# Performance work log

Measured on AMD Instinct MI355X. Metric: run time of the kernel, lower is better.

## Reference

```python
import jax, jax.numpy as jnp
import numpy as np

D_MODEL = 1024
NUM_HEADS = 16
HEAD_DIM = D_MODEL // NUM_HEADS
SCALE = HEAD_DIM ** -0.5
ROPE_BASE = 10000.0


def _rope_cos_sin(seq_len, dim, dtype=jnp.float32):
    inv_freq = 1.0 / (ROPE_BASE ** (jnp.arange(0, dim, 2, dtype=jnp.float32) / dim))
    t = jnp.arange(seq_len, dtype=jnp.float32)
    freqs = t[:, None] * inv_freq[None, :]            # [S, dim/2]
    emb = jnp.concatenate([freqs, freqs], axis=-1)    # [S, dim]
    # broadcast shape [1, S, 1, dim] to apply over [B, S, H, dim]
    return emb.astype(dtype)[None, :, None, :]


def _rotate_half(x):
    half = x.shape[-1] // 2
    x1, x2 = x[..., :half], x[..., half:]
    return jnp.concatenate([-x2, x1], axis=-1)


def setup_inputs() -> dict:
    key = jax.random.key(0)
    ks = jax.random.split(key, 5)
    B, S = 2, 2048
    x = jax.random.normal(ks[0], (B, S, D_MODEL), dtype=jnp.float32)
    wq = jax.random.normal(ks[1], (D_MODEL, D_MODEL), dtype=jnp.float32) * (D_MODEL ** -0.5)
    wk = jax.random.normal(ks[2], (D_MODEL, D_MODEL), dtype=jnp.float32) * (D_MODEL ** -0.5)
    wv = jax.random.normal(ks[3], (D_MODEL, D_MODEL), dtype=jnp.float32) * (D_MODEL ** -0.5)
    wo = jax.random.normal(ks[4], (D_MODEL, D_MODEL), dtype=jnp.float32) * (D_MODEL ** -0.5)
    attention_mask = jnp.tril(jnp.ones((S, S), dtype=jnp.int32))  # causal
    return {"x": x, "wq": wq, "wk": wk, "wv": wv, "wo": wo,
            "attention_mask": attention_mask}


def reference(x, wq, wk, wv, wo, attention_mask):
    B, S, _ = x.shape
    # projections (nn.Linear, no bias: y = x @ W^T)
    q = (x @ wq.T).reshape(B, S, NUM_HEADS, HEAD_DIM)
    k = (x @ wk.T).reshape(B, S, NUM_HEADS, HEAD_DIM)
    v = (x @ wv.T).reshape(B, S, NUM_HEADS, HEAD_DIM)
    # RoPE
    emb = _rope_cos_sin(S, HEAD_DIM, x.dtype)
    cos, sin = jnp.cos(emb), jnp.sin(emb)
    q = q * cos + _rotate_half(q) * sin
    k = k * cos + _rotate_half(k) * sin
    # attention scores [B, H, S, S]
    scores = jnp.einsum('bihd,bjhd->bhij', q, k) * SCALE
    mask = attention_mask[None, None, :, :]  # 2D mask -> broadcast over batch, heads
    scores = jnp.where(mask == 0, -jnp.inf, scores)
    attn = jax.nn.softmax(scores, axis=-1)
    attn = jnp.nan_to_num(attn, nan=0.0)  # fully-masked rows -> 0
    out = jnp.einsum('bhij,bjhd->bihd', attn, v).reshape(B, S, D_MODEL)
    return out @ wo.T
```

## Files before the change

kernel.cpp:

```cpp
#include <hip/hip_runtime.h>

typedef __bf16 bf16;
typedef __attribute__((ext_vector_type(8))) __bf16 bf16x8;
typedef __attribute__((ext_vector_type(4))) float f32x4;
typedef __attribute__((ext_vector_type(4))) short s16x4;
typedef __attribute__((ext_vector_type(4))) unsigned u32x4;

#define SEQ 2048
#define DM 1024
#define NH 16
#define HD 64
#define QSCALE 0.1803368801111204f

static __device__ __forceinline__ void gl_lds16(const bf16* g, bf16* l) {
  __builtin_amdgcn_global_load_lds(
      (const __attribute__((address_space(1))) void*)g,
      (__attribute__((address_space(3))) void*)l, 16, 0, 0);
}

static __device__ __forceinline__ f32x4 mfma16(bf16x8 a, bf16x8 b, f32x4 c) {
  return __builtin_amdgcn_mfma_f32_16x16x32_bf16(a, b, c, 0, 0, 0);
}

static __device__ __forceinline__ unsigned cvt_pk_bf16(float lo, float hi) {
  unsigned r;
  asm("v_cvt_pk_bf16_f32 %0, %1, %2" : "=v"(r) : "v"(lo), "v"(hi));
  return r;
}

static __device__ __forceinline__ float vmax4(f32x4 v) {
  return fmaxf(fmaxf(v[0], v[1]), fmaxf(v[2], v[3]));
}

__global__ __launch_bounds__(256)
void prep_k(const float* __restrict__ x, const float* __restrict__ wq,
            const float* __restrict__ wk, const float* __restrict__ wv,
            const float* __restrict__ wo, bf16* __restrict__ xb,
            bf16* __restrict__ wb, float* __restrict__ tab) {
  int i = blockIdx.x * 256 + threadIdx.x;
  if (i < 2097152) {
    const float* src;
    bf16* dst;
    int j;
    if (i < 1048576) {
      src = x; dst = xb; j = i;
    } else {
      j = i - 1048576;
      int seg = j >> 18;
      src = (seg == 0) ? wq : (seg == 1) ? wk : (seg == 2) ? wv : wo;
      dst = wb;
      src -= (size_t)seg << 20;
    }
    f32x4 v = ((const f32x4*)src)[j];
    s16x4 o;
#pragma unroll
    for (int q = 0; q < 4; ++q) o[q] = __builtin_bit_cast(short, (bf16)v[q]);
    ((s16x4*)dst)[j] = o;
  } else {
    int idx = i - 2097152;
    int s = idx >> 5, j = idx & 31;
    float inv = powf(10000.0f, -(float)j * (1.0f / 32.0f));
    float f = (float)s * inv;
    tab[idx * 2] = cosf(f);
    tab[idx * 2 + 1] = sinf(f);
  }
}

__global__ __launch_bounds__(256)
void gemm_qkv(const bf16* __restrict__ A, const bf16* __restrict__ B,
              bf16* __restrict__ qh, bf16* __restrict__ kh, bf16* __restrict__ vt,
              const float2* __restrict__ tab) {
  const int K = 1024;
  __shared__ __attribute__((aligned(16))) bf16 As[128 * 32];
  __shared__ __attribute__((aligned(16))) bf16 Bs[128 * 32];
  const int t = threadIdx.x;
  const int wv = t >> 6, ln = t & 63, lr = ln & 15, lg = ln >> 4;
  const int wr = wv >> 1, wc = wv & 1;
  const int m0 = blockIdx.y * 128, n0 = blockIdx.x * 128;
  const int srow = t >> 2, sslot = t & 3;
  const int seg = n0 >> 10;
  const int hh = ((n0 & 1023) + wc * 64) >> 6;

  f32x4 acc[4][4] = {};

  for (int kt = 0; kt < K; kt += 32) {
#pragma unroll
    for (int c = 0; c < 2; ++c) {
      int row = srow + (c << 6);
      int lsl = sslot ^ (row & 3);
      gl_lds16(A + (size_t)(m0 + row) * K + kt + lsl * 8, As + c * 2048 + wv * 512);
      gl_lds16(B + (size_t)(n0 + row) * K + kt + lsl * 8, Bs + c * 2048 + wv * 512);
    }
    __syncthreads();
    bf16x8 af[4], bfr[4];
#pragma unroll
    for (int i = 0; i < 4; ++i) {
      int ra = wr * 64 + i * 16 + lr;
      af[i] = *(const bf16x8*)(As + ra * 32 + ((lg ^ (ra & 3)) << 3));
      int rb = wc * 64 + i * 16 + lr;
      bfr[i] = *(const bf16x8*)(Bs + rb * 32 + ((lg ^ (rb & 3)) << 3));
    }
#pragma unroll
    for (int i = 0; i < 4; ++i)
#pragma unroll
      for (int j = 0; j < 4; ++j)
        acc[i][j] = mfma16(af[i], bfr[j], acc[i][j]);
    __syncthreads();
  }

#pragma unroll
  for (int i = 0; i < 4; ++i) {
    int row0 = m0 + wr * 64 + i * 16 + lg * 4;
    int bb = row0 >> 11, s0r = row0 & (SEQ - 1);
    if (seg < 2) {
      bf16* dst = (seg == 0) ? qh : kh;
      float scl = (seg == 0) ? QSCALE : 1.0f;
      size_t base = ((size_t)(bb * NH + hh) * SEQ + s0r) * HD;
#pragma unroll
      for (int j = 0; j < 2; ++j) {
        int dlo = j * 16 + lr;
#pragma unroll
        for (int r = 0; r < 4; ++r) {
          float2 cs = tab[(size_t)(s0r + r) * 32 + dlo];
          float a = acc[i][j][r], b2 = acc[i][j + 2][r];
          float na = (a * cs.x - b2 * cs.y) * scl;
          float nb = (b2 * cs.x + a * cs.y) * scl;
          dst[base + (size_t)r * HD + dlo] = (bf16)na;
          dst[base + (size_t)r * HD + dlo + 32] = (bf16)nb;
        }
      }
    } else {
#pragma unroll
      for (int j = 0; j < 4; ++j) {
        int d = j * 16 + lr;
        s16x4 pk;
#pragma unroll
        for (int r = 0; r < 4; ++r) pk[r] = __builtin_bit_cast(short, (bf16)acc[i][j][r]);
        *(s16x4*)(vt + ((size_t)(bb * NH + hh) * HD + d) * SEQ + s0r) = pk;
      }
    }
  }
}

__global__ __launch_bounds__(256)
void gemm_bt_f32(const bf16* __restrict__ A, const bf16* __restrict__ B,
                 float* __restrict__ C, int M, int N, int K) {
  __shared__ __attribute__((aligned(16))) bf16 As[128 * 32];
  __shared__ __attribute__((aligned(16))) bf16 Bs[128 * 32];
  const int t = threadIdx.x;
  const int wv = t >> 6, ln = t & 63, lr = ln & 15, lg = ln >> 4;
  const int wr = wv >> 1, wc = wv & 1;
  const int m0 = blockIdx.y * 128, n0 = blockIdx.x * 128;
  const int srow = t >> 2, sslot = t & 3;

  f32x4 acc[4][4] = {};

  for (int kt = 0; kt < K; kt += 32) {
#pragma unroll
    for (int c = 0; c < 2; ++c) {
      int row = srow + (c << 6);
      int lsl = sslot ^ (row & 3);
      gl_lds16(A + (size_t)(m0 + row) * K + kt + lsl * 8, As + c * 2048 + wv * 512);
      gl_lds16(B + (size_t)(n0 + row) * K + kt + lsl * 8, Bs + c * 2048 + wv * 512);
    }
    __syncthreads();
    bf16x8 af[4], bfr[4];
#pragma unroll
    for (int i = 0; i < 4; ++i) {
      int ra = wr * 64 + i * 16 + lr;
      af[i] = *(const bf16x8*)(As + ra * 32 + ((lg ^ (ra & 3)) << 3));
      int rb = wc * 64 + i * 16 + lr;
      bfr[i] = *(const bf16x8*)(Bs + rb * 32 + ((lg ^ (rb & 3)) << 3));
    }
#pragma unroll
    for (int i = 0; i < 4; ++i)
#pragma unroll
      for (int j = 0; j < 4; ++j)
        acc[i][j] = mfma16(af[i], bfr[j], acc[i][j]);
    __syncthreads();
  }

#pragma unroll
  for (int i = 0; i < 4; ++i) {
    int row0 = m0 + wr * 64 + i * 16 + lg * 4;
#pragma unroll
    for (int j = 0; j < 4; ++j) {
      int col = n0 + wc * 64 + j * 16 + lr;
#pragma unroll
      for (int r = 0; r < 4; ++r)
        C[(size_t)(row0 + r) * N + col] = acc[i][j][r];
    }
  }
}

template <bool MASKED>
static __device__ __forceinline__ void attn_tile_lds(
    const bf16* Ksb, const bf16* Vsb, unsigned* plw,
    const bf16x8* qf, f32x4* acc, float& m_run, float& l_run,
    int lr, int lg, int qrow, int s0) {
  f32x4 sc[4] = {};
#pragma unroll
  for (int fi = 0; fi < 4; ++fi) {
    int row = fi * 16 + lr;
    int sw = row & 7;
    bf16x8 k0 = *(const bf16x8*)(Ksb + row * 64 + ((lg ^ sw) << 3));
    bf16x8 k1 = *(const bf16x8*)(Ksb + row * 64 + (((4 + lg) ^ sw) << 3));
    sc[fi] = mfma16(k0, qf[0], sc[fi]);
    sc[fi] = mfma16(k1, qf[1], sc[fi]);
  }
  bf16x8 vf[2][4];
#pragma unroll
  for (int kc = 0; kc < 2; ++kc)
#pragma unroll
    for (int d0 = 0; d0 < 4; ++d0) {
      int row = d0 * 16 + lr;
      int sw = row & 7;
      vf[kc][d0] = *(const bf16x8*)(Vsb + row * 64 + (((kc * 4 + lg) ^ sw) << 3));
    }
  if (MASKED) {
#pragma unroll
    for (int fi = 0; fi < 4; ++fi)
#pragma unroll
      for (int r = 0; r < 4; ++r) {
        int kv = s0 + fi * 16 + lg * 4 + r;
        sc[fi][r] = (kv <= qrow) ? sc[fi][r] : -3e38f;
      }
  }
  float mx = fmaxf(fmaxf(vmax4(sc[0]), vmax4(sc[1])),
                   fmaxf(vmax4(sc[2]), vmax4(sc[3])));
  mx = fmaxf(mx, __shfl_xor(mx, 16));
  mx = fmaxf(mx, __shfl_xor(mx, 32));
  if (!__all(mx <= m_run)) {
    float mn = fmaxf(m_run, mx);
    float alpha = __builtin_amdgcn_exp2f(m_run - mn);
    m_run = mn;
    l_run *= alpha;
#pragma unroll
    for (int d0 = 0; d0 < 4; ++d0)
#pragma unroll
      for (int r = 0; r < 4; ++r) acc[d0][r] *= alpha;
  }
  float pf[4][4], sm = 0.0f;
#pragma unroll
  for (int fi = 0; fi < 4; ++fi)
#pragma unroll
    for (int r = 0; r < 4; ++r) {
      pf[fi][r] = __builtin_amdgcn_exp2f(sc[fi][r] - m_run);
      sm += pf[fi][r];
    }
  sm += __shfl_xor(sm, 16);
  sm += __shfl_xor(sm, 32);
  l_run += sm;

  const int sw2 = (lr & 7) << 2;
#pragma unroll
  for (int fi = 0; fi < 4; ++fi)
#pragma unroll
    for (int hh = 0; hh < 2; ++hh)
      plw[lr * 32 + ((fi * 8 + lg * 2 + hh) ^ sw2)] =
          cvt_pk_bf16(pf[fi][2 * hh], pf[fi][2 * hh + 1]);
  asm volatile("s_waitcnt lgkmcnt(0)" ::: "memory");
#pragma unroll
  for (int kc = 0; kc < 2; ++kc) {
    u32x4 praw = *(const u32x4*)(plw + lr * 32 + ((kc * 16 + lg * 4) ^ sw2));
    bf16x8 pb = __builtin_bit_cast(bf16x8, praw);
#pragma unroll
    for (int d0 = 0; d0 < 4; ++d0)
      acc[d0] = mfma16(vf[kc][d0], pb, acc[d0]);
  }
  asm volatile("" ::: "memory");
}

__global__ __launch_bounds__(256, 4)
void attn_k(const bf16* __restrict__ qh, const bf16* __restrict__ kh,
            const bf16* __restrict__ vt, bf16* __restrict__ ao) {
  __shared__ __attribute__((aligned(16))) bf16 Ks[2][64 * 64];
  __shared__ __attribute__((aligned(16))) bf16 Vs[2][64 * 64];
  __shared__ __attribute__((aligned(16))) unsigned plds[4][512];

  const int t = threadIdx.x, wv = t >> 6, ln = t & 63, lr = ln & 15, lg = ln >> 4;
  const int bid = blockIdx.x;
  const int xcd = bid & 7, g = bid >> 3;
  const int bh = xcd * 4 + (g & 3);
  const int s_ = (g >> 2) & 7, k_ = g >> 5;
  const int qt = (k_ == 0) ? (31 - s_) : (k_ == 1) ? (16 + s_) : (k_ == 2) ? (15 - s_) : s_;
  const int b = bh >> 4, h = bh & 15;

  const bf16* qp = qh + (size_t)bh * SEQ * HD;
  const bf16* kp = kh + (size_t)bh * SEQ * HD;
  const bf16* vp = vt + (size_t)bh * HD * SEQ;
  unsigned* plw = &plds[wv][0];

  const int qrow = qt * 64 + wv * 16 + lr;

  bf16x8 qf[2];
  qf[0] = *(const bf16x8*)(qp + (size_t)qrow * HD + lg * 8);
  qf[1] = *(const bf16x8*)(qp + (size_t)qrow * HD + 32 + lg * 8);

  f32x4 acc[4] = {};
  float m_run = -3e38f, l_run = 0.0f;

  const int nt = qt + 1;

  auto STAGE = [&](int buf, int tt) {
    int s0 = tt * 64;
#pragma unroll
    for (int c = 0; c < 2; ++c) {
      int rA = wv * 16 + c * 8;
      int row = rA + (ln >> 3);
      int sl = (ln & 7) ^ (row & 7);
      gl_lds16(kp + (size_t)(s0 + row) * HD + (sl << 3), &Ks[buf][rA * 64]);
      gl_lds16(vp + (size_t)row * SEQ + s0 + (sl << 3), &Vs[buf][rA * 64]);
    }
  };

  STAGE(0, 0);
  asm volatile("s_waitcnt vmcnt(0)" ::: "memory");
  __builtin_amdgcn_s_barrier();

  int cur = 0;
  for (int tt = 0; tt < nt; ++tt) {
    if (tt + 1 < nt) STAGE(cur ^ 1, tt + 1);
    if (tt == qt)
      attn_tile_lds<true>(&Ks[cur][0], &Vs[cur][0], plw, qf, acc, m_run, l_run,
                          lr, lg, qrow, tt * 64);
    else
      attn_tile_lds<false>(&Ks[cur][0], &Vs[cur][0], plw, qf, acc, m_run, l_run,
                           lr, lg, qrow, tt * 64);
    asm volatile("s_waitcnt vmcnt(0)" ::: "memory");
    __builtin_amdgcn_s_barrier();
    cur ^= 1;
  }

  float invl = 1.0f / l_run;
  bf16* aop = ao + ((size_t)b * SEQ + qrow) * DM + h * HD;
#pragma unroll
  for (int d0 = 0; d0 < 4; ++d0) {
    unsigned lo = cvt_pk_bf16(acc[d0][0] * invl, acc[d0][1] * invl);
    unsigned hi = cvt_pk_bf16(acc[d0][2] * invl, acc[d0][3] * invl);
    uint2 pk; pk.x = lo; pk.y = hi;
    *(uint2*)(aop + d0 * 16 + lg * 4) = pk;
  }
}

extern "C" void kernel_launch(void* const* d_in, const int* in_sizes, int n_in,
                              void* d_out, int out_size, void* d_ws, size_t ws_size,
                              hipStream_t stream) {
  const float* x = (const float*)d_in[0];
  const float* wq = (const float*)d_in[1];
  const float* wk = (const float*)d_in[2];
  const float* wv = (const float*)d_in[3];
  const float* wo = (const float*)d_in[4];

  char* ws = (char*)d_ws;
  const size_t MB = 1ull << 20;
  bf16* xb    = (bf16*)ws;
  bf16* wqkvb = (bf16*)(ws + 8 * MB);
  bf16* wob   = (bf16*)(ws + 14 * MB);
  bf16* qhb   = (bf16*)(ws + 16 * MB);
  bf16* khb   = (bf16*)(ws + 24 * MB);
  bf16* vtb   = (bf16*)(ws + 32 * MB);
  float* tab  = (float*)(ws + 40 * MB);
  bf16* aob = xb;

  prep_k<<<8448, 256, 0, stream>>>(x, wq, wk, wv, wo, xb, wqkvb, tab);

  gemm_qkv<<<dim3(24, 32), 256, 0, stream>>>(xb, wqkvb, qhb, khb, vtb, (const float2*)tab);

  attn_k<<<1024, 256, 0, stream>>>(qhb, khb, vtb, aob);

  gemm_bt_f32<<<dim3(8, 32), 256, 0, stream>>>(aob, wob, (float*)d_out, 4096, 1024, 1024);
}
```

Measured before the change: 121.5 us.

## Load V directly from global, add MFMA priority hints, remap GEMM and attention block order

The attention kernel stops staging V tiles through LDS. Each lane now loads its V fragments straight from global memory at the start of each tile, which removes half the LDS traffic and footprint but adds per-wave global loads with no cross-wave reuse. It also wraps the MFMA sections in s_setprio and a sched_barrier, and replaces the balanced query-tile ordering with a simple longest-first order. Both GEMM kernels remap block IDs so that consecutive hardware blocks land on the same XCD, aiming for better L2 locality.

```diff
diff --git a/kernel.cpp b/kernel.cpp
--- a/kernel.cpp
+++ b/kernel.cpp
@@ -76,7 +76,9 @@
   const int t = threadIdx.x;
   const int wv = t >> 6, ln = t & 63, lr = ln & 15, lg = ln >> 4;
   const int wr = wv >> 1, wc = wv & 1;
-  const int m0 = blockIdx.y * 128, n0 = blockIdx.x * 128;
+  const int l_hw = blockIdx.x + 24 * blockIdx.y;
+  const int lid = (l_hw & 7) * 96 + (l_hw >> 3);
+  const int m0 = (lid / 24) * 128, n0 = (lid % 24) * 128;
   const int srow = t >> 2, sslot = t & 3;
   const int seg = n0 >> 10;
   const int hh = ((n0 & 1023) + wc * 64) >> 6;
@@ -150,7 +152,9 @@
   const int t = threadIdx.x;
   const int wv = t >> 6, ln = t & 63, lr = ln & 15, lg = ln >> 4;
   const int wr = wv >> 1, wc = wv & 1;
-  const int m0 = blockIdx.y * 128, n0 = blockIdx.x * 128;
+  const int l_hw = blockIdx.x + 8 * blockIdx.y;
+  const int lid = (l_hw & 7) * 32 + (l_hw >> 3);
+  const int m0 = (lid >> 3) * 128, n0 = (lid & 7) * 128;
   const int srow = t >> 2, sslot = t & 3;
 
   f32x4 acc[4][4] = {};
@@ -195,10 +199,17 @@
 
 template <bool MASKED>
 static __device__ __forceinline__ void attn_tile_lds(
-    const bf16* Ksb, const bf16* Vsb, unsigned* plw,
+    const bf16* Ksb, const bf16* vp_l, unsigned* plw,
     const bf16x8* qf, f32x4* acc, float& m_run, float& l_run,
     int lr, int lg, int qrow, int s0) {
+  bf16x8 vf[2][4];
+#pragma unroll
+  for (int kc = 0; kc < 2; ++kc)
+#pragma unroll
+    for (int d0 = 0; d0 < 4; ++d0)
+      vf[kc][d0] = *(const bf16x8*)(vp_l + (size_t)(d0 * 16) * SEQ + s0 + kc * 32);
   f32x4 sc[4] = {};
+  __builtin_amdgcn_s_setprio(1);
 #pragma unroll
   for (int fi = 0; fi < 4; ++fi) {
     int row = fi * 16 + lr;
@@ -208,15 +219,7 @@
     sc[fi] = mfma16(k0, qf[0], sc[fi]);
     sc[fi] = mfma16(k1, qf[1], sc[fi]);
   }
-  bf16x8 vf[2][4];
-#pragma unroll
-  for (int kc = 0; kc < 2; ++kc)
-#pragma unroll
-    for (int d0 = 0; d0 < 4; ++d0) {
-      int row = d0 * 16 + lr;
-      int sw = row & 7;
-      vf[kc][d0] = *(const bf16x8*)(Vsb + row * 64 + (((kc * 4 + lg) ^ sw) << 3));
-    }
+  __builtin_amdgcn_s_setprio(0);
   if (MASKED) {
 #pragma unroll
     for (int fi = 0; fi < 4; ++fi)
@@ -260,6 +263,8 @@
       plw[lr * 32 + ((fi * 8 + lg * 2 + hh) ^ sw2)] =
           cvt_pk_bf16(pf[fi][2 * hh], pf[fi][2 * hh + 1]);
   asm volatile("s_waitcnt lgkmcnt(0)" ::: "memory");
+  __builtin_amdgcn_sched_barrier(0);
+  __builtin_amdgcn_s_setprio(1);
 #pragma unroll
   for (int kc = 0; kc < 2; ++kc) {
     u32x4 praw = *(const u32x4*)(plw + lr * 32 + ((kc * 16 + lg * 4) ^ sw2));
@@ -268,6 +273,7 @@
     for (int d0 = 0; d0 < 4; ++d0)
       acc[d0] = mfma16(vf[kc][d0], pb, acc[d0]);
   }
+  __builtin_amdgcn_s_setprio(0);
   asm volatile("" ::: "memory");
 }
 
@@ -275,20 +281,18 @@
 void attn_k(const bf16* __restrict__ qh, const bf16* __restrict__ kh,
             const bf16* __restrict__ vt, bf16* __restrict__ ao) {
   __shared__ __attribute__((aligned(16))) bf16 Ks[2][64 * 64];
-  __shared__ __attribute__((aligned(16))) bf16 Vs[2][64 * 64];
   __shared__ __attribute__((aligned(16))) unsigned plds[4][512];
 
   const int t = threadIdx.x, wv = t >> 6, ln = t & 63, lr = ln & 15, lg = ln >> 4;
   const int bid = blockIdx.x;
   const int xcd = bid & 7, g = bid >> 3;
   const int bh = xcd * 4 + (g & 3);
-  const int s_ = (g >> 2) & 7, k_ = g >> 5;
-  const int qt = (k_ == 0) ? (31 - s_) : (k_ == 1) ? (16 + s_) : (k_ == 2) ? (15 - s_) : s_;
+  const int qt = 31 - (g >> 2);
   const int b = bh >> 4, h = bh & 15;
 
   const bf16* qp = qh + (size_t)bh * SEQ * HD;
   const bf16* kp = kh + (size_t)bh * SEQ * HD;
-  const bf16* vp = vt + (size_t)bh * HD * SEQ;
+  const bf16* vp_l = vt + (size_t)bh * HD * SEQ + (size_t)lr * SEQ + lg * 8;
   unsigned* plw = &plds[wv][0];
 
   const int qrow = qt * 64 + wv * 16 + lr;
@@ -310,7 +314,6 @@
       int row = rA + (ln >> 3);
       int sl = (ln & 7) ^ (row & 7);
       gl_lds16(kp + (size_t)(s0 + row) * HD + (sl << 3), &Ks[buf][rA * 64]);
-      gl_lds16(vp + (size_t)row * SEQ + s0 + (sl << 3), &Vs[buf][rA * 64]);
     }
   };
 
@@ -322,10 +325,10 @@
   for (int tt = 0; tt < nt; ++tt) {
     if (tt + 1 < nt) STAGE(cur ^ 1, tt + 1);
     if (tt == qt)
-      attn_tile_lds<true>(&Ks[cur][0], &Vs[cur][0], plw, qf, acc, m_run, l_run,
+      attn_tile_lds<true>(&Ks[cur][0], vp_l, plw, qf, acc, m_run, l_run,
                           lr, lg, qrow, tt * 64);
     else
-      attn_tile_lds<false>(&Ks[cur][0], &Vs[cur][0], plw, qf, acc, m_run, l_run,
+      attn_tile_lds<false>(&Ks[cur][0], vp_l, plw, qf, acc, m_run, l_run,
                            lr, lg, qrow, tt * 64);
     asm volatile("s_waitcnt vmcnt(0)" ::: "memory");
     __builtin_amdgcn_s_barrier();
```

Measured after the change: 162.5 us. 33.8% more time.
